# Performance work log

Hardware: AMD Instinct MI355X
Metric: run time of the kernel (lower is better)

The kernel has to match this reference:

```python
import jax, jax.numpy as jnp
import numpy as np

B, T, V, E, H, M, L = 64, 512, 32000, 256, 600, 600, 4


def _lstm_dir(x, Wih, Whh, b, reverse):
    # x: [T,B,Din]; PyTorch gate order i,f,g,o; b = b_ih + b_hh fused
    Hd = Whh.shape[1]
    Bn = x.shape[1]

    def step(carry, xt):
        h, c = carry
        g = xt @ Wih.T + h @ Whh.T + b
        i, f, gg, o = jnp.split(g, 4, axis=-1)
        c = jax.nn.sigmoid(f) * c + jax.nn.sigmoid(i) * jnp.tanh(gg)
        h = jax.nn.sigmoid(o) * jnp.tanh(c)
        return (h, c), h

    init = (jnp.zeros((Bn, Hd), x.dtype), jnp.zeros((Bn, Hd), x.dtype))
    _, hs = jax.lax.scan(step, init, x, reverse=reverse)
    return hs  # [T,B,H]


def _crf_log_likelihood(emissions, tags, transitions, start_trans, end_trans):
    # emissions [B,T,L], tags [B,T]; full-length mask
    emit_sc = jnp.take_along_axis(emissions, tags[..., None], axis=-1)[..., 0].sum(-1)
    trans_sc = transitions[tags[:, :-1], tags[:, 1:]].sum(-1)
    numerator = start_trans[tags[:, 0]] + emit_sc + trans_sc + end_trans[tags[:, -1]]

    alpha0 = start_trans[None, :] + emissions[:, 0]  # [B,L]

    def step(alpha, e_t):
        a = jax.nn.logsumexp(alpha[:, :, None] + transitions[None], axis=1) + e_t
        return a, None

    alpha, _ = jax.lax.scan(step, alpha0, jnp.swapaxes(emissions, 0, 1)[1:])
    denominator = jax.nn.logsumexp(alpha + end_trans[None, :], axis=1)
    return (numerator - denominator).sum()


def _viterbi(emissions, transitions, start_trans, end_trans):
    alpha0 = start_trans[None, :] + emissions[:, 0]

    def step(alpha, e_t):
        sc = alpha[:, :, None] + transitions[None]  # [B,L,L]
        bp = jnp.argmax(sc, axis=1)                 # [B,L]
        return jnp.max(sc, axis=1) + e_t, bp

    alpha, bps = jax.lax.scan(step, alpha0, jnp.swapaxes(emissions, 0, 1)[1:])
    last = jnp.argmax(alpha + end_trans[None, :], axis=1)  # [B]

    def back(tag, bp):
        prev = jnp.take_along_axis(bp, tag[:, None], axis=1)[:, 0]
        return prev, tag

    first, tags_rev = jax.lax.scan(back, last, bps, reverse=True)
    return jnp.concatenate([first[:, None], jnp.swapaxes(tags_rev, 0, 1)], axis=1)


def setup_inputs() -> dict:
    key = jax.random.key(0)
    ks = jax.random.split(key, 24)
    s = 0.05
    d = {}
    d['us'] = jax.random.randint(ks[0], (B, T), 0, V)
    d['ls'] = jax.random.randint(ks[1], (B, T), 0, L)
    d['embed'] = jax.random.normal(ks[2], (V, E), jnp.float32) * s
    # layer 0 (input E), layer 1 (input 2H); f=forward dir, b=backward dir
    d['Wih0f'] = jax.random.normal(ks[3], (4 * H, E), jnp.float32) * s
    d['Whh0f'] = jax.random.normal(ks[4], (4 * H, H), jnp.float32) * s
    d['b0f'] = jnp.zeros((4 * H,), jnp.float32)
    d['Wih0b'] = jax.random.normal(ks[5], (4 * H, E), jnp.float32) * s
    d['Whh0b'] = jax.random.normal(ks[6], (4 * H, H), jnp.float32) * s
    d['b0b'] = jnp.zeros((4 * H,), jnp.float32)
    d['Wih1f'] = jax.random.normal(ks[7], (4 * H, 2 * H), jnp.float32) * s
    d['Whh1f'] = jax.random.normal(ks[8], (4 * H, H), jnp.float32) * s
    d['b1f'] = jnp.zeros((4 * H,), jnp.float32)
    d['Wih1b'] = jax.random.normal(ks[9], (4 * H, 2 * H), jnp.float32) * s
    d['Whh1b'] = jax.random.normal(ks[10], (4 * H, H), jnp.float32) * s
    d['b1b'] = jnp.zeros((4 * H,), jnp.float32)
    d['W1'] = jax.random.normal(ks[11], (2 * H, M), jnp.float32) * s
    d['bm1'] = jnp.zeros((M,), jnp.float32)
    d['W2'] = jax.random.normal(ks[12], (M, L), jnp.float32) * s
    d['bm2'] = jnp.zeros((L,), jnp.float32)
    d['transitions'] = jax.random.normal(ks[13], (L, L), jnp.float32) * s
    d['start_trans'] = jax.random.normal(ks[14], (L,), jnp.float32) * s
    d['end_trans'] = jax.random.normal(ks[15], (L,), jnp.float32) * s
    return d


def reference(us, ls, embed, Wih0f, Whh0f, b0f, Wih0b, Whh0b, b0b,
              Wih1f, Whh1f, b1f, Wih1b, Whh1b, b1b,
              W1, bm1, W2, bm2, transitions, start_trans, end_trans):
    x = embed[us]                      # [B,T,E] embedding lookup (dropout p=0)
    x = jnp.swapaxes(x, 0, 1)          # [T,B,E]
    h0 = jnp.concatenate([
        _lstm_dir(x, Wih0f, Whh0f, b0f, False),
        _lstm_dir(x, Wih0b, Whh0b, b0b, True)], axis=-1)   # [T,B,2H]
    h1 = jnp.concatenate([
        _lstm_dir(h0, Wih1f, Whh1f, b1f, False),
        _lstm_dir(h0, Wih1b, Whh1b, b1b, True)], axis=-1)  # [T,B,2H]
    ys = (h1 @ W1 + bm1) @ W2 + bm2    # MLP with Identity activation -> [T,B,L]
    ys = jnp.swapaxes(ys, 0, 1)        # [B,T,L]
    ll = _crf_log_likelihood(ys, ls, transitions, start_trans, end_trans)
    loss = -ll / B
    tags = _viterbi(ys, transitions, start_trans, end_trans)
    return loss, tags
```

## Files before the change

### kernel.cpp

```cpp
#include <hip/hip_runtime.h>
#include <hip/hip_bf16.h>
#include <math.h>

#define T_ 512
#define B_ 64
#define E_ 256
#define H_ 600
#define G4 2400
#define MTOT 32768
#define NP 2432
#define KP1 1216
#define GSTR (38 * 19 * 512)
#define PARS (2 * 64 * 608)

typedef __attribute__((ext_vector_type(8))) short bf16x8;
typedef __attribute__((ext_vector_type(4))) float f32x4;

static __device__ __forceinline__ ushort f2bf(float x) {
    unsigned u = __builtin_bit_cast(unsigned, x);
    unsigned r = (u + 0x7FFFu + ((u >> 16) & 1u)) >> 16;
    return (ushort)r;
}
static __device__ __forceinline__ float bf2f(ushort h) {
    unsigned u = ((unsigned)h) << 16;
    return __builtin_bit_cast(float, u);
}

__global__ __launch_bounds__(256) void zero_kernel(float* __restrict__ p, int n) {
    int i = blockIdx.x * 256 + threadIdx.x;
    if (i < n) p[i] = 0.f;
}

__global__ __launch_bounds__(256) void xsplit(const int* __restrict__ us,
                                              const float* __restrict__ embed,
                                              ushort* __restrict__ xh) {
    int m = blockIdx.x;
    int t = m >> 6, b = m & 63;
    int tok = us[b * T_ + t];
    int k = threadIdx.x;
    float v = embed[(size_t)tok * E_ + k];
    xh[(size_t)m * E_ + k] = f2bf(v);
}

__global__ __launch_bounds__(256) void padzero(ushort* __restrict__ h) {
    int idx = blockIdx.x * 256 + threadIdx.x;
    int m = idx >> 4, c = 1200 + (idx & 15);
    h[(size_t)m * KP1 + c] = 0;
}

__global__ __launch_bounds__(512) void pack_wih(const float* __restrict__ Wf,
                                                const float* __restrict__ Wb, int K, int NKS,
                                                ushort* __restrict__ phF,
                                                ushort* __restrict__ phB) {
    int nb = blockIdx.x, ks = blockIdx.y, dz = blockIdx.z;
    const float* W = dz ? Wb : Wf;
    ushort* ph = dz ? phB : phF;
    int tid = threadIdx.x;
    int l = tid >> 3, e = tid & 7;
    int g = nb / 38, ub = nb % 38;
    int u = ub * 16 + (l & 15);
    int k = ks * 32 + (l >> 4) * 8 + e;
    float v = (u < 600 && k < K) ? W[(size_t)(g * 600 + u) * K + k] : 0.f;
    ph[((size_t)nb * NKS + ks) * 512 + tid] = f2bf(v);
}

__global__ __launch_bounds__(512) void pack_whh(
    const float* __restrict__ W0f, const float* __restrict__ W0b,
    const float* __restrict__ W1f, const float* __restrict__ W1b,
    ushort* __restrict__ pwh, ushort* __restrict__ pwl) {
    int ub = blockIdx.x, ks = blockIdx.y, ld = blockIdx.z;
    const float* W = (ld == 0) ? W0f : (ld == 1) ? W0b : (ld == 2) ? W1f : W1b;
    int tid = threadIdx.x;
    int l = tid >> 3, e = tid & 7;
    int u = ub * 16 + (l & 15);
    int k = ks * 32 + (l >> 4) * 8 + e;
#pragma unroll
    for (int g = 0; g < 4; ++g) {
        float v = (u < 600 && k < 600) ? W[(size_t)(g * 600 + u) * 600 + k] : 0.f;
        ushort hi = f2bf(v);
        size_t o = ((((size_t)ld * 4 + g) * 38 + ub) * 19 + ks) * 512 + tid;
        pwh[o] = hi;
        pwl[o] = f2bf(v - bf2f(hi));
    }
}

__global__ __launch_bounds__(64) void packbias(const float* __restrict__ b0f,
                                               const float* __restrict__ b0b,
                                               const float* __restrict__ b1f,
                                               const float* __restrict__ b1b,
                                               float* __restrict__ bfr) {
    int ub = blockIdx.x, g = blockIdx.y, ld = blockIdx.z;
    const float* b = (ld == 0) ? b0f : (ld == 1) ? b0b : (ld == 2) ? b1f : b1b;
    int lane = threadIdx.x;
    float4 v;
    float* vp = (float*)&v;
#pragma unroll
    for (int r = 0; r < 4; ++r) {
        int u = ub * 16 + (lane >> 4) * 4 + r;
        vp[r] = (u < 600) ? b[g * 600 + u] : 0.f;
    }
    *(float4*)&bfr[((((size_t)ld * 4 + g) * 38 + ub) * 64 + lane) * 4] = v;
}

__global__ void wc_kernel(const float* __restrict__ W1, const float* __restrict__ bm1,
                          const float* __restrict__ W2, const float* __restrict__ bm2,
                          float* __restrict__ Wc, float* __restrict__ bc) {
    int idx = blockIdx.x * 256 + threadIdx.x;
    if (idx < 4800) {
        int k = idx >> 2, l = idx & 3;
        float acc = 0.f;
        for (int j = 0; j < 600; ++j) acc += W1[(size_t)k * 600 + j] * W2[j * 4 + l];
        Wc[idx] = acc;
    }
    if (idx < 4) {
        float acc = bm2[idx];
        for (int j = 0; j < 600; ++j) acc += bm1[j] * W2[j * 4 + idx];
        bc[idx] = acc;
    }
}

#define LOADAG(Ah, KS)                                                           \
    _Pragma("unroll") for (int i = 0; i < 4; ++i) {                              \
        size_t o = ((size_t)(wn16 + i) * NKS + (KS)) * 512 + lane * 8;           \
        Ah[i] = *(const bf16x8*)(Aph + o);                                       \
    }
#define READB(BUF)                                                               \
    _Pragma("unroll") for (int j = 0; j < 4; ++j) {                              \
        bh[j] = *(const bf16x8*)&BsH[BUF][wm + j * 16 + fr][kb8];                \
    }
#define MFALL(Ah)                                                                \
    _Pragma("unroll") for (int i = 0; i < 4; ++i)                                \
        _Pragma("unroll") for (int j = 0; j < 4; ++j)                            \
            acc[i][j] = __builtin_amdgcn_mfma_f32_16x16x32_bf16(Ah[i], bh[j], acc[i][j], 0, 0, 0);

__global__ __launch_bounds__(256) void gemm_mfma(
    const ushort* __restrict__ AphF, const ushort* __restrict__ AphB,
    const ushort* __restrict__ actH,
    int Kp, int NKS, int m_offF, int m_offB,
    float* __restrict__ preF, float* __restrict__ preB) {
    __shared__ __align__(16) ushort BsH[2][128][40];
    const ushort* Aph = blockIdx.z ? AphB : AphF;
    float* preX = blockIdx.z ? preB : preF;
    int m_off = blockIdx.z ? m_offB : m_offF;
    int n0 = blockIdx.x * 128, m0 = blockIdx.y * 128;
    int tid = threadIdx.x, lane = tid & 63, w = tid >> 6;
    int wn16 = (n0 >> 4) + (w >> 1) * 4;
    int wm = (w & 1) * 64;
    int fr = lane & 15, kb8 = (lane >> 4) * 8;
    int srow = tid >> 1, skg = (tid & 1) * 16;
    const ushort* bHrow = actH + (size_t)(m_off + m0 + srow) * Kp + skg;

    uint4 rh0 = *(const uint4*)bHrow, rh1 = *(const uint4*)(bHrow + 8);

    bf16x8 a0h[4], a1h[4], bh[4];
    LOADAG(a0h, 0)

    f32x4 acc[4][4] = {};

    for (int ks = 0; ks < NKS; ks += 2) {
        *(uint4*)&BsH[0][srow][skg] = rh0;
        *(uint4*)&BsH[0][srow][skg + 8] = rh1;
        {
            const ushort* bh_ = bHrow + (ks + 1) * 32;
            rh0 = *(const uint4*)bh_; rh1 = *(const uint4*)(bh_ + 8);
        }
        LOADAG(a1h, ks + 1)
        __syncthreads();
        READB(0)
        MFALL(a0h)
        __syncthreads();
        *(uint4*)&BsH[1][srow][skg] = rh0;
        *(uint4*)&BsH[1][srow][skg + 8] = rh1;
        {
            int ksn = (ks + 2 < NKS) ? ks + 2 : 0;
            const ushort* bh_ = bHrow + ksn * 32;
            rh0 = *(const uint4*)bh_; rh1 = *(const uint4*)(bh_ + 8);
            LOADAG(a0h, ksn)
        }
        __syncthreads();
        READB(1)
        MFALL(a1h)
        __syncthreads();
    }

#pragma unroll
    for (int i = 0; i < 4; ++i) {
        int n16 = wn16 + i;
        int g = n16 / 38, ub = n16 - g * 38;
#pragma unroll
        for (int j = 0; j < 4; ++j) {
            int mloc = m0 + wm + j * 16;
            int tl = mloc >> 6, ntg = (mloc >> 4) & 3;
            float* dst = preX + (((((size_t)tl * 4 + g) * 38 + ub) * 4 + ntg) * 64 + lane) * 4;
            *(f32x4*)dst = acc[i][j];
        }
    }
}

#define LOADA(Ah, Al, KS)                                                        \
    _Pragma("unroll") for (int g = 0; g < 4; ++g) {                              \
        size_t o = (size_t)(dir * 4 + g) * GSTR + wub + (size_t)(KS)*512 + lane * 8; \
        Ah[g] = *(const bf16x8*)(pwh + o);                                       \
        Al[g] = *(const bf16x8*)(pwl + o);                                       \
    }
#define LOADB1(Bh, Bl, KS)                                                       \
    {                                                                            \
        size_t o = (size_t)(KS)*32 + fk8;                                        \
        Bh = *(const bf16x8*)(hHb + o);                                          \
        Bl = *(const bf16x8*)(hLb + o);                                          \
    }
#define MFT1(Aa, Bb)                                                             \
    _Pragma("unroll") for (int g = 0; g < 4; ++g)                                \
        acc[g] = __builtin_amdgcn_mfma_f32_16x16x32_bf16(Aa[g], Bb, acc[g], 0, 0, 0);
#define MF31(Ah, Al, Bh, Bl) MFT1(Ah, Bh) MFT1(Ah, Bl) MFT1(Al, Bh)

__global__ __launch_bounds__(256) void lstm_step_mfma(
    const ushort* __restrict__ pwh, const ushort* __restrict__ pwl,
    const ushort* __restrict__ hInH, const ushort* __restrict__ hInL,
    ushort* __restrict__ hOutH, ushort* __restrict__ hOutL,
    const float* __restrict__ preF2, const float* __restrict__ preB2,
    int tF, int tB,
    const float* __restrict__ biasFr, int layer,
    float* __restrict__ cQ,
    ushort* __restrict__ h0H, int mF, int mB,
    float* __restrict__ h1f, float* __restrict__ h1b, int oF, int oB, int chunkRows) {
    __shared__ float hsh[4][16][17];
    int tid = threadIdx.x;
    int lane = tid & 63, nt = tid >> 6;
    int blk = blockIdx.x;
    int dir = (blk >= 38) ? 1 : 0;
    int ub = blk - dir * 38;
    int u16 = ub * 16;
    int frow = lane & 15, rr = lane >> 4, fk8 = rr * 8;
    size_t wub = (size_t)ub * 9728;
    const ushort* hHb = hInH + ((size_t)dir * 64 + nt * 16 + frow) * 608;
    const ushort* hLb = hInL + ((size_t)dir * 64 + nt * 16 + frow) * 608;

    f32x4 acc[4] = {};
    bf16x8 A0h[4], A0l[4], A1h[4], A1l[4];
    bf16x8 B0h, B0l, B1h, B1l;

    LOADA(A0h, A0l, 0)
    LOADB1(B0h, B0l, 0)
    for (int ks = 0; ks < 18; ks += 2) {
        LOADA(A1h, A1l, ks + 1)
        LOADB1(B1h, B1l, ks + 1)
        MF31(A0h, A0l, B0h, B0l)
        LOADA(A0h, A0l, ks + 2)
        LOADB1(B0h, B0l, ks + 2)
        MF31(A1h, A1l, B1h, B1l)
    }
    MF31(A0h, A0l, B0h, B0l)

    const float* preX = dir ? preB2 : preF2;
    int t = dir ? tB : tF;
    float4 pg[4], bf4[4];
#pragma unroll
    for (int g = 0; g < 4; ++g) {
        pg[g] = *(const float4*)(preX + (((((size_t)t * 4 + g) * 38 + ub) * 4 + nt) * 64 + lane) * 4);
        bf4[g] = *(const float4*)(biasFr + ((((size_t)(layer * 2 + dir) * 4 + g) * 38 + ub) * 64 + lane) * 4);
    }
    int slot = (dir * 38 + ub) * 4 + nt;
    float* cslot = cQ + ((size_t)slot * 64 + lane) * 4;
    float4 cvec = *(float4*)cslot;
    float* cvp = (float*)&cvec;
#pragma unroll
    for (int r = 0; r < 4; ++r) {
        int u = u16 + rr * 4 + r;
        bool valid = (u < 600);
        float gi, gf, gg, go;
        if (valid) {
            gi = acc[0][r] + ((float*)&pg[0])[r] + ((float*)&bf4[0])[r];
            gf = acc[1][r] + ((float*)&pg[1])[r] + ((float*)&bf4[1])[r];
            gg = acc[2][r] + ((float*)&pg[2])[r] + ((float*)&bf4[2])[r];
            go = acc[3][r] + ((float*)&pg[3])[r] + ((float*)&bf4[3])[r];
        } else {
            gi = gf = gg = go = 0.f;
        }
        float cv = cvp[r];
        float si = 1.f / (1.f + expf(-gi));
        float sf = 1.f / (1.f + expf(-gf));
        float so = 1.f / (1.f + expf(-go));
        float cn = sf * cv + si * tanhf(gg);
        float hn = so * tanhf(cn);
        cvp[r] = cn;
        hsh[nt][frow][rr * 4 + r] = hn;
    }
    *(float4*)cslot = cvec;
    __syncthreads();

    {
        int bl = lane >> 2, q = lane & 3;
        int b = nt * 16 + bl;
        float v0 = hsh[nt][bl][q * 4 + 0], v1 = hsh[nt][bl][q * 4 + 1];
        float v2 = hsh[nt][bl][q * 4 + 2], v3 = hsh[nt][bl][q * 4 + 3];
        ushort h0_ = f2bf(v0), h1_ = f2bf(v1), h2_ = f2bf(v2), h3_ = f2bf(v3);
        ushort4 hv = {h0_, h1_, h2_, h3_};
        ushort4 lv = {f2bf(v0 - bf2f(h0_)), f2bf(v1 - bf2f(h1_)),
                      f2bf(v2 - bf2f(h2_)), f2bf(v3 - bf2f(h3_))};
        size_t ho = ((size_t)dir * 64 + b) * 608 + u16 + q * 4;
        *(ushort4*)&hOutH[ho] = hv;
        *(ushort4*)&hOutL[ho] = lv;
        if (layer == 0 && (u16 + q * 4 < 600)) {
            size_t so_ = (size_t)((dir ? mB : mF) + b) * KP1 + dir * 600 + u16 + q * 4;
            *(ushort4*)&h0H[so_] = hv;
        }
    }
    if (layer == 1) {
        int u_l = lane & 15, br = (lane >> 4) * 4;
        if (u16 + u_l < 600) {
            float4 hv;
            hv.x = hsh[nt][br + 0][u_l];
            hv.y = hsh[nt][br + 1][u_l];
            hv.z = hsh[nt][br + 2][u_l];
            hv.w = hsh[nt][br + 3][u_l];
            float* op = dir ? h1b : h1f;
            *(float4*)&op[(size_t)(u16 + u_l) * chunkRows + (dir ? oB : oF) + nt * 16 + br] = hv;
        }
    }
}

__global__ __launch_bounds__(256) void emis_add(const float* __restrict__ h1C, int cols,
                                                const float* __restrict__ Wc,
                                                const float* __restrict__ bc, int addBias,
                                                float* __restrict__ ys, int t0) {
    int lane = threadIdx.x & 63;
    int l = __builtin_amdgcn_readfirstlane(threadIdx.x >> 6);
    int tl = blockIdx.x;
    float acc = addBias ? bc[l] : 0.f;
    for (int k = 0; k < H_; ++k)
        acc = fmaf(h1C[(size_t)k * cols + tl * 64 + lane], Wc[k * 4 + l], acc);
    int t = t0 + tl, b = lane;
    ys[((size_t)b * T_ + t) * 4 + l] += acc;
}

__global__ void crf_fwd(const float* __restrict__ ys, const int* __restrict__ ls,
                        const float* __restrict__ trans, const float* __restrict__ startT,
                        const float* __restrict__ endT, float* __restrict__ llb) {
    int b = blockIdx.x;
    int lane = threadIdx.x;
    float acc = 0.f;
    for (int t = lane; t < T_; t += 64) {
        int tg = ls[b * T_ + t];
        acc += ys[((size_t)b * T_ + t) * 4 + tg];
        if (t > 0) acc += trans[ls[b * T_ + t - 1] * 4 + tg];
    }
    for (int off = 32; off; off >>= 1) acc += __shfl_down(acc, off);
    float num = 0.f;
    if (lane == 0) num = startT[ls[b * T_]] + acc + endT[ls[b * T_ + T_ - 1]];

    float a = -1e30f;
    if (lane < 4) a = startT[lane] + ys[((size_t)b * T_) * 4 + lane];
    for (int t = 1; t < T_; ++t) {
        float a0 = __shfl(a, 0), a1 = __shfl(a, 1), a2 = __shfl(a, 2), a3 = __shfl(a, 3);
        if (lane < 4) {
            float v0 = a0 + trans[0 * 4 + lane];
            float v1 = a1 + trans[1 * 4 + lane];
            float v2 = a2 + trans[2 * 4 + lane];
            float v3 = a3 + trans[3 * 4 + lane];
            float mx = fmaxf(fmaxf(v0, v1), fmaxf(v2, v3));
            float ssum = expf(v0 - mx) + expf(v1 - mx) + expf(v2 - mx) + expf(v3 - mx);
            a = mx + logf(ssum) + ys[((size_t)b * T_ + t) * 4 + lane];
        }
    }
    float a0 = __shfl(a, 0), a1 = __shfl(a, 1), a2 = __shfl(a, 2), a3 = __shfl(a, 3);
    if (lane == 0) {
        float v0 = a0 + endT[0], v1 = a1 + endT[1], v2 = a2 + endT[2], v3 = a3 + endT[3];
        float mx = fmaxf(fmaxf(v0, v1), fmaxf(v2, v3));
        float den = mx + logf(expf(v0 - mx) + expf(v1 - mx) + expf(v2 - mx) + expf(v3 - mx));
        llb[b] = num - den;
    }
}

__global__ void final_loss(const float* __restrict__ llb, float* __restrict__ out) {
    int lane = threadIdx.x;
    float v = llb[lane];
    for (int off = 32; off; off >>= 1) v += __shfl_down(v, off);
    if (lane == 0) out[0] = -v / 64.0f;
}

__global__ void viterbi(const float* __restrict__ ys, const float* __restrict__ trans,
                        const float* __restrict__ startT, const float* __restrict__ endT,
                        float* __restrict__ out) {
    __shared__ unsigned char bp[T_ * 4];
    int b = blockIdx.x;
    int lane = threadIdx.x;
    float a = -1e30f;
    if (lane < 4) a = startT[lane] + ys[((size_t)b * T_) * 4 + lane];
    for (int t = 1; t < T_; ++t) {
        float a0 = __shfl(a, 0), a1 = __shfl(a, 1), a2 = __shfl(a, 2), a3 = __shfl(a, 3);
        if (lane < 4) {
            float av[4] = {a0, a1, a2, a3};
            float best = av[0] + trans[lane];
            int bi = 0;
            for (int lp = 1; lp < 4; ++lp) {
                float v = av[lp] + trans[lp * 4 + lane];
                if (v > best) { best = v; bi = lp; }
            }
            bp[t * 4 + lane] = (unsigned char)bi;
            a = best + ys[((size_t)b * T_ + t) * 4 + lane];
        }
    }
    float a0 = __shfl(a, 0), a1 = __shfl(a, 1), a2 = __shfl(a, 2), a3 = __shfl(a, 3);
    if (lane == 0) {
        float v[4] = {a0 + endT[0], a1 + endT[1], a2 + endT[2], a3 + endT[3]};
        int tag = 0;
        float best = v[0];
        for (int l = 1; l < 4; ++l)
            if (v[l] > best) { best = v[l]; tag = l; }
        out[1 + b * T_ + (T_ - 1)] = (float)tag;
        for (int t = T_ - 1; t >= 1; --t) {
            tag = bp[t * 4 + tag];
            out[1 + b * T_ + t - 1] = (float)tag;
        }
    }
}

extern "C" void kernel_launch(void* const* d_in, const int* in_sizes, int n_in,
                              void* d_out, int out_size, void* d_ws, size_t ws_size,
                              hipStream_t stream) {
    const int* us = (const int*)d_in[0];
    const int* ls = (const int*)d_in[1];
    const float* embed = (const float*)d_in[2];
    const float* Wih0f = (const float*)d_in[3];
    const float* Whh0f = (const float*)d_in[4];
    const float* b0f   = (const float*)d_in[5];
    const float* Wih0b = (const float*)d_in[6];
    const float* Whh0b = (const float*)d_in[7];
    const float* b0b   = (const float*)d_in[8];
    const float* Wih1f = (const float*)d_in[9];
    const float* Whh1f = (const float*)d_in[10];
    const float* b1f   = (const float*)d_in[11];
    const float* Wih1b = (const float*)d_in[12];
    const float* Whh1b = (const float*)d_in[13];
    const float* b1b   = (const float*)d_in[14];
    const float* W1    = (const float*)d_in[15];
    const float* bm1   = (const float*)d_in[16];
    const float* W2    = (const float*)d_in[17];
    const float* bm2   = (const float*)d_in[18];
    const float* trans = (const float*)d_in[19];
    const float* startT= (const float*)d_in[20];
    const float* endT  = (const float*)d_in[21];
    float* out = (float*)d_out;

    char* p = (char*)d_ws;
    auto alloc = [&](size_t bytes) {
        char* r = p;
        p += (bytes + 255) & ~(size_t)255;
        return r;
    };
    ushort* xspH = (ushort*)alloc((size_t)MTOT * E_ * 2);
    ushort* h0spH = (ushort*)alloc((size_t)MTOT * KP1 * 2);
    ushort* pw0hf = (ushort*)alloc((size_t)152 * 8 * 512 * 2);
    ushort* pw0hb = (ushort*)alloc((size_t)152 * 8 * 512 * 2);
    ushort* pw1hf = (ushort*)alloc((size_t)152 * 38 * 512 * 2);
    ushort* pw1hb = (ushort*)alloc((size_t)152 * 38 * 512 * 2);
    ushort* pwh = (ushort*)alloc((size_t)16 * GSTR * 2);
    ushort* pwl = (ushort*)alloc((size_t)16 * GSTR * 2);
    ushort* hTh = (ushort*)alloc((size_t)2 * PARS * 2);
    ushort* hTl = (ushort*)alloc((size_t)2 * PARS * 2);
    float* cQ  = (float*)alloc((size_t)304 * 64 * 4 * 4);
    float* biasFr = (float*)alloc((size_t)4 * 4 * 38 * 64 * 4 * 4);
    float* Wc  = (float*)alloc(4800 * 4);
    float* bc  = (float*)alloc(4 * 4);
    float* ysb = (float*)alloc((size_t)B_ * T_ * 4 * 4);
    float* llb = (float*)alloc(64 * 4);

    size_t used = (size_t)(p - (char*)d_ws);
    size_t perTc = (size_t)2 * 2432 * 64 * 4 + (size_t)2 * H_ * 64 * 4;
    int Tc = 128;
    while (Tc > 8 && used + (size_t)Tc * perTc + 4096 > ws_size) Tc >>= 1;
    float* preF = (float*)alloc((size_t)Tc * 2432 * 64 * 4);
    float* preB = (float*)alloc((size_t)Tc * 2432 * 64 * 4);
    float* h1fC = (float*)alloc((size_t)H_ * Tc * 64 * 4);
    float* h1bC = (float*)alloc((size_t)H_ * Tc * 64 * 4);
    int nc = T_ / Tc;
    int chunkRows = Tc * 64;

    xsplit<<<MTOT, 256, 0, stream>>>(us, embed, xspH);
    pack_wih<<<dim3(152, 8, 2), 512, 0, stream>>>(Wih0f, Wih0b, E_, 8, pw0hf, pw0hb);
    pack_wih<<<dim3(152, 38, 2), 512, 0, stream>>>(Wih1f, Wih1b, 1200, 38, pw1hf, pw1hb);
    pack_whh<<<dim3(38, 19, 4), 512, 0, stream>>>(Whh0f, Whh0b, Whh1f, Whh1b, pwh, pwl);
    packbias<<<dim3(38, 4, 4), 64, 0, stream>>>(b0f, b0b, b1f, b1b, biasFr);
    padzero<<<(MTOT * 16) / 256, 256, 0, stream>>>(h0spH);
    wc_kernel<<<19, 256, 0, stream>>>(W1, bm1, W2, bm2, Wc, bc);
    zero_kernel<<<(B_ * T_ * 4 + 255) / 256, 256, 0, stream>>>(ysb, B_ * T_ * 4);

    for (int layer = 0; layer < 2; ++layer) {
        int Kp = layer ? KP1 : E_;
        int NKS = Kp / 32;
        const ushort* aH = layer ? h0spH : xspH;
        const ushort* AphF = layer ? pw1hf : pw0hf;
        const ushort* AphB = layer ? pw1hb : pw0hb;
        const ushort* pwhL = pwh + (size_t)layer * 8 * GSTR;
        const ushort* pwlL = pwl + (size_t)layer * 8 * GSTR;

        zero_kernel<<<(PARS + 255) / 256, 256, 0, stream>>>((float*)hTh, PARS);
        zero_kernel<<<(PARS + 255) / 256, 256, 0, stream>>>((float*)hTl, PARS);
        zero_kernel<<<(304 * 64 * 4 + 255) / 256, 256, 0, stream>>>(cQ, 304 * 64 * 4);

        for (int c = 0; c < nc; ++c) {
            int moffF = c * Tc * 64;
            int moffB = (T_ - (c + 1) * Tc) * 64;
            dim3 gg(NP / 128, chunkRows / 128, 2);
            gemm_mfma<<<gg, 256, 0, stream>>>(AphF, AphB, aH, Kp, NKS, moffF, moffB,
                                              preF, preB);
            for (int s = 0; s < Tc; ++s) {
                int step = c * Tc + s;
                int par = step & 1;
                lstm_step_mfma<<<76, 256, 0, stream>>>(
                    pwhL, pwlL,
                    hTh + (size_t)par * PARS, hTl + (size_t)par * PARS,
                    hTh + (size_t)(par ^ 1) * PARS, hTl + (size_t)(par ^ 1) * PARS,
                    preF, preB, s, Tc - 1 - s,
                    biasFr, layer, cQ,
                    h0spH, step * 64, (T_ - 1 - step) * 64,
                    h1fC, h1bC, s * 64, (Tc - 1 - s) * 64, chunkRows);
            }
            if (layer == 1) {
                emis_add<<<Tc, 256, 0, stream>>>(h1fC, chunkRows, Wc, bc, 1, ysb, c * Tc);
                emis_add<<<Tc, 256, 0, stream>>>(h1bC, chunkRows, Wc + 600 * 4, bc, 0, ysb,
                                                 T_ - (c + 1) * Tc);
            }
        }
    }

    crf_fwd<<<B_, 64, 0, stream>>>(ysb, ls, trans, startT, endT, llb);
    final_loss<<<1, 64, 0, stream>>>(llb, out);
    viterbi<<<B_, 64, 0, stream>>>(ysb, trans, startT, endT, out);
}
```

Measured before the change: 15.02 ms.

## Fuse per-step LSTM launches into a persistent cooperative kernel with LDS-resident weights

Replaces the one-launch-per-timestep LSTM recurrence with a single cooperative kernel per chunk. It loops over timesteps and separates them with grid.sync, and it loads each block's recurrent weight slice into shared memory once instead of re-reading it from global memory every step. The cell state stays in registers across the chunk, and the MFMA loop gets a deeper software-pipelined prefetch. The aim is to remove kernel launch overhead and repeated weight traffic. The cost is heavy LDS use (about 150KB per block) and grid-wide barrier latency, which requires all 76 blocks to be co-resident.

```diff
diff --git a/kernel.cpp b/kernel.cpp
--- a/kernel.cpp
+++ b/kernel.cpp
@@ -1,6 +1,9 @@
 #include <hip/hip_runtime.h>
 #include <hip/hip_bf16.h>
+#include <hip/hip_cooperative_groups.h>
 #include <math.h>
+
+namespace cg = cooperative_groups;
 
 #define T_ 512
 #define B_ 64
@@ -197,34 +200,37 @@
     }
 }
 
-#define LOADA(Ah, Al, KS)                                                        \
+#define CC_LOADA(SL, KS)                                                         \
     _Pragma("unroll") for (int g = 0; g < 4; ++g) {                              \
-        size_t o = (size_t)(dir * 4 + g) * GSTR + wub + (size_t)(KS)*512 + lane * 8; \
-        Ah[g] = *(const bf16x8*)(pwh + o);                                       \
-        Al[g] = *(const bf16x8*)(pwl + o);                                       \
-    }
-#define LOADB1(Bh, Bl, KS)                                                       \
+        Ah[SL][g] = *(const bf16x8*)&wlds[0][g][(size_t)(KS)*512 + lane * 8];    \
+        Al[SL][g] = *(const bf16x8*)&wlds[1][g][(size_t)(KS)*512 + lane * 8];    \
+    }
+#define CC_LOADB(SL, KS)                                                         \
     {                                                                            \
-        size_t o = (size_t)(KS)*32 + fk8;                                        \
-        Bh = *(const bf16x8*)(hHb + o);                                          \
-        Bl = *(const bf16x8*)(hLb + o);                                          \
-    }
-#define MFT1(Aa, Bb)                                                             \
+        Bh[SL] = *(const bf16x8*)(hHb + (size_t)(KS)*32 + fk8);                  \
+        Bl[SL] = *(const bf16x8*)(hLb + (size_t)(KS)*32 + fk8);                  \
+    }
+#define CC_MF3(SA, SB)                                                           \
     _Pragma("unroll") for (int g = 0; g < 4; ++g)                                \
-        acc[g] = __builtin_amdgcn_mfma_f32_16x16x32_bf16(Aa[g], Bb, acc[g], 0, 0, 0);
-#define MF31(Ah, Al, Bh, Bl) MFT1(Ah, Bh) MFT1(Ah, Bl) MFT1(Al, Bh)
-
-__global__ __launch_bounds__(256) void lstm_step_mfma(
+        acc[g] = __builtin_amdgcn_mfma_f32_16x16x32_bf16(Ah[SA][g], Bh[SB], acc[g], 0, 0, 0); \
+    _Pragma("unroll") for (int g = 0; g < 4; ++g)                                \
+        acc[g] = __builtin_amdgcn_mfma_f32_16x16x32_bf16(Ah[SA][g], Bl[SB], acc[g], 0, 0, 0); \
+    _Pragma("unroll") for (int g = 0; g < 4; ++g)                                \
+        acc[g] = __builtin_amdgcn_mfma_f32_16x16x32_bf16(Al[SA][g], Bh[SB], acc[g], 0, 0, 0);
+
+__global__ __launch_bounds__(256, 1) void lstm_chunk_coop(
     const ushort* __restrict__ pwh, const ushort* __restrict__ pwl,
-    const ushort* __restrict__ hInH, const ushort* __restrict__ hInL,
-    ushort* __restrict__ hOutH, ushort* __restrict__ hOutL,
+    ushort* __restrict__ hTh, ushort* __restrict__ hTl,
     const float* __restrict__ preF2, const float* __restrict__ preB2,
-    int tF, int tB,
+    int Tc, int step0,
     const float* __restrict__ biasFr, int layer,
     float* __restrict__ cQ,
-    ushort* __restrict__ h0H, int mF, int mB,
-    float* __restrict__ h1f, float* __restrict__ h1b, int oF, int oB, int chunkRows) {
+    ushort* __restrict__ h0H,
+    float* __restrict__ h1f, float* __restrict__ h1b, int chunkRows) {
+    __shared__ ushort wlds[2][4][19 * 512];
     __shared__ float hsh[4][16][17];
+    cg::grid_group grid = cg::this_grid();
+
     int tid = threadIdx.x;
     int lane = tid & 63, nt = tid >> 6;
     int blk = blockIdx.x;
@@ -232,92 +238,120 @@
     int ub = blk - dir * 38;
     int u16 = ub * 16;
     int frow = lane & 15, rr = lane >> 4, fk8 = rr * 8;
-    size_t wub = (size_t)ub * 9728;
-    const ushort* hHb = hInH + ((size_t)dir * 64 + nt * 16 + frow) * 608;
-    const ushort* hLb = hInL + ((size_t)dir * 64 + nt * 16 + frow) * 608;
-
-    f32x4 acc[4] = {};
-    bf16x8 A0h[4], A0l[4], A1h[4], A1l[4];
-    bf16x8 B0h, B0l, B1h, B1l;
-
-    LOADA(A0h, A0l, 0)
-    LOADB1(B0h, B0l, 0)
-    for (int ks = 0; ks < 18; ks += 2) {
-        LOADA(A1h, A1l, ks + 1)
-        LOADB1(B1h, B1l, ks + 1)
-        MF31(A0h, A0l, B0h, B0l)
-        LOADA(A0h, A0l, ks + 2)
-        LOADB1(B0h, B0l, ks + 2)
-        MF31(A1h, A1l, B1h, B1l)
-    }
-    MF31(A0h, A0l, B0h, B0l)
+
+#pragma unroll
+    for (int g = 0; g < 4; ++g) {
+        const uint4* sH = (const uint4*)(pwh + (size_t)(dir * 4 + g) * GSTR + (size_t)ub * 9728);
+        const uint4* sL = (const uint4*)(pwl + (size_t)(dir * 4 + g) * GSTR + (size_t)ub * 9728);
+        uint4* dH = (uint4*)&wlds[0][g][0];
+        uint4* dL = (uint4*)&wlds[1][g][0];
+        for (int i = tid; i < 1216; i += 256) {
+            dH[i] = sH[i];
+            dL[i] = sL[i];
+        }
+    }
 
     const float* preX = dir ? preB2 : preF2;
-    int t = dir ? tB : tF;
-    float4 pg[4], bf4[4];
-#pragma unroll
-    for (int g = 0; g < 4; ++g) {
-        pg[g] = *(const float4*)(preX + (((((size_t)t * 4 + g) * 38 + ub) * 4 + nt) * 64 + lane) * 4);
+    float4 bf4[4];
+#pragma unroll
+    for (int g = 0; g < 4; ++g)
         bf4[g] = *(const float4*)(biasFr + ((((size_t)(layer * 2 + dir) * 4 + g) * 38 + ub) * 64 + lane) * 4);
-    }
+
     int slot = (dir * 38 + ub) * 4 + nt;
     float* cslot = cQ + ((size_t)slot * 64 + lane) * 4;
     float4 cvec = *(float4*)cslot;
     float* cvp = (float*)&cvec;
-#pragma unroll
-    for (int r = 0; r < 4; ++r) {
-        int u = u16 + rr * 4 + r;
-        bool valid = (u < 600);
-        float gi, gf, gg, go;
-        if (valid) {
-            gi = acc[0][r] + ((float*)&pg[0])[r] + ((float*)&bf4[0])[r];
-            gf = acc[1][r] + ((float*)&pg[1])[r] + ((float*)&bf4[1])[r];
-            gg = acc[2][r] + ((float*)&pg[2])[r] + ((float*)&bf4[2])[r];
-            go = acc[3][r] + ((float*)&pg[3])[r] + ((float*)&bf4[3])[r];
-        } else {
-            gi = gf = gg = go = 0.f;
-        }
-        float cv = cvp[r];
-        float si = 1.f / (1.f + expf(-gi));
-        float sf = 1.f / (1.f + expf(-gf));
-        float so = 1.f / (1.f + expf(-go));
-        float cn = sf * cv + si * tanhf(gg);
-        float hn = so * tanhf(cn);
-        cvp[r] = cn;
-        hsh[nt][frow][rr * 4 + r] = hn;
+    __syncthreads();
+
+    for (int s = 0; s < Tc; ++s) {
+        int par = (step0 + s) & 1;
+        const ushort* hHb = hTh + (size_t)par * PARS + ((size_t)dir * 64 + nt * 16 + frow) * 608;
+        const ushort* hLb = hTl + (size_t)par * PARS + ((size_t)dir * 64 + nt * 16 + frow) * 608;
+        int t = dir ? (Tc - 1 - s) : s;
+
+        float4 pg[4];
+#pragma unroll
+        for (int g = 0; g < 4; ++g)
+            pg[g] = *(const float4*)(preX + (((((size_t)t * 4 + g) * 38 + ub) * 4 + nt) * 64 + lane) * 4);
+
+        f32x4 acc[4] = {};
+        bf16x8 Ah[3][4], Al[3][4], Bh[6], Bl[6];
+        CC_LOADB(0, 0) CC_LOADB(1, 1) CC_LOADB(2, 2)
+        CC_LOADB(3, 3) CC_LOADB(4, 4) CC_LOADB(5, 5)
+        CC_LOADA(0, 0) CC_LOADA(1, 1)
+#pragma unroll
+        for (int ks = 0; ks < 19; ++ks) {
+            const int ca = ks % 3, cb = ks % 6;
+            if (ks + 2 < 19) {
+                const int pa = (ks + 2) % 3;
+                CC_LOADA(pa, ks + 2)
+            }
+            if (ks + 6 < 19) {
+                const int pb = (ks + 6) % 6;
+                CC_LOADB(pb, ks + 6)
+            }
+            CC_MF3(ca, cb)
+        }
+
+#pragma unroll
+        for (int r = 0; r < 4; ++r) {
+            int u = u16 + rr * 4 + r;
+            bool valid = (u < 600);
+            float gi, gf, gg, go;
+            if (valid) {
+                gi = acc[0][r] + ((float*)&pg[0])[r] + ((float*)&bf4[0])[r];
+                gf = acc[1][r] + ((float*)&pg[1])[r] + ((float*)&bf4[1])[r];
+                gg = acc[2][r] + ((float*)&pg[2])[r] + ((float*)&bf4[2])[r];
+                go = acc[3][r] + ((float*)&pg[3])[r] + ((float*)&bf4[3])[r];
+            } else {
+                gi = gf = gg = go = 0.f;
+            }
+            float cv = cvp[r];
+            float si = 1.f / (1.f + expf(-gi));
+            float sf = 1.f / (1.f + expf(-gf));
+            float so = 1.f / (1.f + expf(-go));
+            float cn = sf * cv + si * tanhf(gg);
+            float hn = so * tanhf(cn);
+            cvp[r] = cn;
+            hsh[nt][frow][rr * 4 + r] = hn;
+        }
+        __syncthreads();
+        {
+            int step = step0 + s;
+            int mF = step * 64, mB = (T_ - 1 - step) * 64;
+            int bl = lane >> 2, q = lane & 3;
+            int b = nt * 16 + bl;
+            float v0 = hsh[nt][bl][q * 4 + 0], v1 = hsh[nt][bl][q * 4 + 1];
+            float v2 = hsh[nt][bl][q * 4 + 2], v3 = hsh[nt][bl][q * 4 + 3];
+            ushort h0_ = f2bf(v0), h1_ = f2bf(v1), h2_ = f2bf(v2), h3_ = f2bf(v3);
+            ushort4 hv = {h0_, h1_, h2_, h3_};
+            ushort4 lv = {f2bf(v0 - bf2f(h0_)), f2bf(v1 - bf2f(h1_)),
+                          f2bf(v2 - bf2f(h2_)), f2bf(v3 - bf2f(h3_))};
+            size_t ho = (size_t)(par ^ 1) * PARS + ((size_t)dir * 64 + b) * 608 + u16 + q * 4;
+            *(ushort4*)&hTh[ho] = hv;
+            *(ushort4*)&hTl[ho] = lv;
+            if (layer == 0 && (u16 + q * 4 < 600)) {
+                size_t so_ = (size_t)((dir ? mB : mF) + b) * KP1 + dir * 600 + u16 + q * 4;
+                *(ushort4*)&h0H[so_] = hv;
+            }
+        }
+        if (layer == 1) {
+            int oF = s * 64, oB = (Tc - 1 - s) * 64;
+            int u_l = lane & 15, br = (lane >> 4) * 4;
+            if (u16 + u_l < 600) {
+                float4 hv;
+                hv.x = hsh[nt][br + 0][u_l];
+                hv.y = hsh[nt][br + 1][u_l];
+                hv.z = hsh[nt][br + 2][u_l];
+                hv.w = hsh[nt][br + 3][u_l];
+                float* op = dir ? h1b : h1f;
+                *(float4*)&op[(size_t)(u16 + u_l) * chunkRows + (dir ? oB : oF) + nt * 16 + br] = hv;
+            }
+        }
+        __syncthreads();
+        if (s != Tc - 1) grid.sync();
     }
     *(float4*)cslot = cvec;
-    __syncthreads();
-
-    {
-        int bl = lane >> 2, q = lane & 3;
-        int b = nt * 16 + bl;
-        float v0 = hsh[nt][bl][q * 4 + 0], v1 = hsh[nt][bl][q * 4 + 1];
-        float v2 = hsh[nt][bl][q * 4 + 2], v3 = hsh[nt][bl][q * 4 + 3];
-        ushort h0_ = f2bf(v0), h1_ = f2bf(v1), h2_ = f2bf(v2), h3_ = f2bf(v3);
-        ushort4 hv = {h0_, h1_, h2_, h3_};
-        ushort4 lv = {f2bf(v0 - bf2f(h0_)), f2bf(v1 - bf2f(h1_)),
-                      f2bf(v2 - bf2f(h2_)), f2bf(v3 - bf2f(h3_))};
-        size_t ho = ((size_t)dir * 64 + b) * 608 + u16 + q * 4;
-        *(ushort4*)&hOutH[ho] = hv;
-        *(ushort4*)&hOutL[ho] = lv;
-        if (layer == 0 && (u16 + q * 4 < 600)) {
-            size_t so_ = (size_t)((dir ? mB : mF) + b) * KP1 + dir * 600 + u16 + q * 4;
-            *(ushort4*)&h0H[so_] = hv;
-        }
-    }
-    if (layer == 1) {
-        int u_l = lane & 15, br = (lane >> 4) * 4;
-        if (u16 + u_l < 600) {
-            float4 hv;
-            hv.x = hsh[nt][br + 0][u_l];
-            hv.y = hsh[nt][br + 1][u_l];
-            hv.z = hsh[nt][br + 2][u_l];
-            hv.w = hsh[nt][br + 3][u_l];
-            float* op = dir ? h1b : h1f;
-            *(float4*)&op[(size_t)(u16 + u_l) * chunkRows + (dir ? oB : oF) + nt * 16 + br] = hv;
-        }
-    }
 }
 
 __global__ __launch_bounds__(256) void emis_add(const float* __restrict__ h1C, int cols,
@@ -505,17 +539,21 @@
             dim3 gg(NP / 128, chunkRows / 128, 2);
             gemm_mfma<<<gg, 256, 0, stream>>>(AphF, AphB, aH, Kp, NKS, moffF, moffB,
                                               preF, preB);
-            for (int s = 0; s < Tc; ++s) {
-                int step = c * Tc + s;
-                int par = step & 1;
-                lstm_step_mfma<<<76, 256, 0, stream>>>(
-                    pwhL, pwlL,
-                    hTh + (size_t)par * PARS, hTl + (size_t)par * PARS,
-                    hTh + (size_t)(par ^ 1) * PARS, hTl + (size_t)(par ^ 1) * PARS,
-                    preF, preB, s, Tc - 1 - s,
-                    biasFr, layer, cQ,
-                    h0spH, step * 64, (T_ - 1 - step) * 64,
-                    h1fC, h1bC, s * 64, (Tc - 1 - s) * 64, chunkRows);
+            {
+                int step0 = c * Tc;
+                const ushort* a0 = pwhL; const ushort* a1 = pwlL;
+                ushort* a2 = hTh; ushort* a3 = hTl;
+                const float* a4 = preF; const float* a5 = preB;
+                int a6 = Tc; int a7 = step0;
+                const float* a8 = biasFr; int a9 = layer;
+                float* a10 = cQ;
+                ushort* a11 = h0spH;
+                float* a12 = h1fC; float* a13 = h1bC;
+                int a14 = chunkRows;
+                void* args[15] = {&a0, &a1, &a2, &a3, &a4, &a5, &a6, &a7,
+                                  &a8, &a9, &a10, &a11, &a12, &a13, &a14};
+                hipLaunchCooperativeKernel((void*)lstm_chunk_coop, dim3(76), dim3(256),
+                                           args, 0, stream);
             }
             if (layer == 1) {
                 emis_add<<<Tc, 256, 0, stream>>>(h1fC, chunkRows, Wc, bc, 1, ysb, c * Tc);
```

New measurement: 19.40 ms. 1.29x slower.

## Store LSTM input-projection and layer-1 outputs in bf16, enlarge chunk size

Applied to the files above, without the earlier changes.

The input-projection GEMM now writes its pre-activations as bf16 instead of fp32, and the LSTM step reads them back as bf16. Layer-1 hidden outputs are also stored as bf16 for the emission kernel. Halving these buffers lets the time chunk grow up to 512, which cuts the number of GEMM launches. The pre-activation and c-state loads are hoisted ahead of the recurrent MFMA loop, and three zeroing launches are merged into one. The cost is reduced precision in the gate pre-activations and emissions, which could shift Viterbi tags.

```diff
diff --git a/kernel.cpp b/kernel.cpp
--- a/kernel.cpp
+++ b/kernel.cpp
@@ -29,6 +29,14 @@
 __global__ __launch_bounds__(256) void zero_kernel(float* __restrict__ p, int n) {
     int i = blockIdx.x * 256 + threadIdx.x;
     if (i < n) p[i] = 0.f;
+}
+
+__global__ __launch_bounds__(256) void zero3(float* __restrict__ a, float* __restrict__ b,
+                                             float* __restrict__ c) {
+    int i = blockIdx.x * 256 + threadIdx.x;
+    a[i] = 0.f;
+    b[i] = 0.f;
+    c[i] = 0.f;
 }
 
 __global__ __launch_bounds__(256) void xsplit(const int* __restrict__ us,
@@ -137,10 +145,10 @@
     const ushort* __restrict__ AphF, const ushort* __restrict__ AphB,
     const ushort* __restrict__ actH,
     int Kp, int NKS, int m_offF, int m_offB,
-    float* __restrict__ preF, float* __restrict__ preB) {
+    ushort* __restrict__ preF, ushort* __restrict__ preB) {
     __shared__ __align__(16) ushort BsH[2][128][40];
     const ushort* Aph = blockIdx.z ? AphB : AphF;
-    float* preX = blockIdx.z ? preB : preF;
+    ushort* preX = blockIdx.z ? preB : preF;
     int m_off = blockIdx.z ? m_offB : m_offF;
     int n0 = blockIdx.x * 128, m0 = blockIdx.y * 128;
     int tid = threadIdx.x, lane = tid & 63, w = tid >> 6;
@@ -191,8 +199,13 @@
         for (int j = 0; j < 4; ++j) {
             int mloc = m0 + wm + j * 16;
             int tl = mloc >> 6, ntg = (mloc >> 4) & 3;
-            float* dst = preX + (((((size_t)tl * 4 + g) * 38 + ub) * 4 + ntg) * 64 + lane) * 4;
-            *(f32x4*)dst = acc[i][j];
+            ushort* dst = preX + (((((size_t)tl * 4 + g) * 38 + ub) * 4 + ntg) * 64 + lane) * 4;
+            ushort4 o;
+            o.x = f2bf(acc[i][j][0]);
+            o.y = f2bf(acc[i][j][1]);
+            o.z = f2bf(acc[i][j][2]);
+            o.w = f2bf(acc[i][j][3]);
+            *(ushort4*)dst = o;
         }
     }
 }
@@ -218,12 +231,12 @@
     const ushort* __restrict__ pwh, const ushort* __restrict__ pwl,
     const ushort* __restrict__ hInH, const ushort* __restrict__ hInL,
     ushort* __restrict__ hOutH, ushort* __restrict__ hOutL,
-    const float* __restrict__ preF2, const float* __restrict__ preB2,
+    const ushort* __restrict__ preF2, const ushort* __restrict__ preB2,
     int tF, int tB,
     const float* __restrict__ biasFr, int layer,
     float* __restrict__ cQ,
     ushort* __restrict__ h0H, int mF, int mB,
-    float* __restrict__ h1f, float* __restrict__ h1b, int oF, int oB, int chunkRows) {
+    ushort* __restrict__ h1f, ushort* __restrict__ h1b, int oF, int oB, int chunkRows) {
     __shared__ float hsh[4][16][17];
     int tid = threadIdx.x;
     int lane = tid & 63, nt = tid >> 6;
@@ -236,6 +249,22 @@
     const ushort* hHb = hInH + ((size_t)dir * 64 + nt * 16 + frow) * 608;
     const ushort* hLb = hInL + ((size_t)dir * 64 + nt * 16 + frow) * 608;
 
+    const ushort* preX = dir ? preB2 : preF2;
+    int t = dir ? tB : tF;
+    ushort4 pgu[4];
+    float4 bf4[4];
+#pragma unroll
+    for (int g = 0; g < 4; ++g) {
+        pgu[g] = *(const ushort4*)(preX +
+            (((((size_t)t * 4 + g) * 38 + ub) * 4 + nt) * 64 + lane) * 4);
+        bf4[g] = *(const float4*)(biasFr +
+            ((((size_t)(layer * 2 + dir) * 4 + g) * 38 + ub) * 64 + lane) * 4);
+    }
+    int slot = (dir * 38 + ub) * 4 + nt;
+    float* cslot = cQ + ((size_t)slot * 64 + lane) * 4;
+    float4 cvec = *(float4*)cslot;
+    float* cvp = (float*)&cvec;
+
     f32x4 acc[4] = {};
     bf16x8 A0h[4], A0l[4], A1h[4], A1l[4];
     bf16x8 B0h, B0l, B1h, B1l;
@@ -252,28 +281,18 @@
     }
     MF31(A0h, A0l, B0h, B0l)
 
-    const float* preX = dir ? preB2 : preF2;
-    int t = dir ? tB : tF;
-    float4 pg[4], bf4[4];
-#pragma unroll
-    for (int g = 0; g < 4; ++g) {
-        pg[g] = *(const float4*)(preX + (((((size_t)t * 4 + g) * 38 + ub) * 4 + nt) * 64 + lane) * 4);
-        bf4[g] = *(const float4*)(biasFr + ((((size_t)(layer * 2 + dir) * 4 + g) * 38 + ub) * 64 + lane) * 4);
-    }
-    int slot = (dir * 38 + ub) * 4 + nt;
-    float* cslot = cQ + ((size_t)slot * 64 + lane) * 4;
-    float4 cvec = *(float4*)cslot;
-    float* cvp = (float*)&cvec;
 #pragma unroll
     for (int r = 0; r < 4; ++r) {
         int u = u16 + rr * 4 + r;
         bool valid = (u < 600);
         float gi, gf, gg, go;
         if (valid) {
-            gi = acc[0][r] + ((float*)&pg[0])[r] + ((float*)&bf4[0])[r];
-            gf = acc[1][r] + ((float*)&pg[1])[r] + ((float*)&bf4[1])[r];
-            gg = acc[2][r] + ((float*)&pg[2])[r] + ((float*)&bf4[2])[r];
-            go = acc[3][r] + ((float*)&pg[3])[r] + ((float*)&bf4[3])[r];
+            const ushort* pp = (const ushort*)&pgu[0];
+            gi = acc[0][r] + bf2f(((const ushort*)&pgu[0])[r]) + ((float*)&bf4[0])[r];
+            gf = acc[1][r] + bf2f(((const ushort*)&pgu[1])[r]) + ((float*)&bf4[1])[r];
+            gg = acc[2][r] + bf2f(((const ushort*)&pgu[2])[r]) + ((float*)&bf4[2])[r];
+            go = acc[3][r] + bf2f(((const ushort*)&pgu[3])[r]) + ((float*)&bf4[3])[r];
+            (void)pp;
         } else {
             gi = gf = gg = go = 0.f;
         }
@@ -309,18 +328,18 @@
     if (layer == 1) {
         int u_l = lane & 15, br = (lane >> 4) * 4;
         if (u16 + u_l < 600) {
-            float4 hv;
-            hv.x = hsh[nt][br + 0][u_l];
-            hv.y = hsh[nt][br + 1][u_l];
-            hv.z = hsh[nt][br + 2][u_l];
-            hv.w = hsh[nt][br + 3][u_l];
-            float* op = dir ? h1b : h1f;
-            *(float4*)&op[(size_t)(u16 + u_l) * chunkRows + (dir ? oB : oF) + nt * 16 + br] = hv;
-        }
-    }
-}
-
-__global__ __launch_bounds__(256) void emis_add(const float* __restrict__ h1C, int cols,
+            ushort4 hv4;
+            hv4.x = f2bf(hsh[nt][br + 0][u_l]);
+            hv4.y = f2bf(hsh[nt][br + 1][u_l]);
+            hv4.z = f2bf(hsh[nt][br + 2][u_l]);
+            hv4.w = f2bf(hsh[nt][br + 3][u_l]);
+            ushort* op = dir ? h1b : h1f;
+            *(ushort4*)&op[(size_t)(u16 + u_l) * chunkRows + (dir ? oB : oF) + nt * 16 + br] = hv4;
+        }
+    }
+}
+
+__global__ __launch_bounds__(256) void emis_add(const ushort* __restrict__ h1C, int cols,
                                                 const float* __restrict__ Wc,
                                                 const float* __restrict__ bc, int addBias,
                                                 float* __restrict__ ys, int t0) {
@@ -329,7 +348,7 @@
     int tl = blockIdx.x;
     float acc = addBias ? bc[l] : 0.f;
     for (int k = 0; k < H_; ++k)
-        acc = fmaf(h1C[(size_t)k * cols + tl * 64 + lane], Wc[k * 4 + l], acc);
+        acc = fmaf(bf2f(h1C[(size_t)k * cols + tl * 64 + lane]), Wc[k * 4 + l], acc);
     int t = t0 + tl, b = lane;
     ys[((size_t)b * T_ + t) * 4 + l] += acc;
 }
@@ -467,13 +486,13 @@
     float* llb = (float*)alloc(64 * 4);
 
     size_t used = (size_t)(p - (char*)d_ws);
-    size_t perTc = (size_t)2 * 2432 * 64 * 4 + (size_t)2 * H_ * 64 * 4;
-    int Tc = 128;
+    size_t perTc = (size_t)2 * 2432 * 64 * 2 + (size_t)2 * H_ * 64 * 2;
+    int Tc = 512;
     while (Tc > 8 && used + (size_t)Tc * perTc + 4096 > ws_size) Tc >>= 1;
-    float* preF = (float*)alloc((size_t)Tc * 2432 * 64 * 4);
-    float* preB = (float*)alloc((size_t)Tc * 2432 * 64 * 4);
-    float* h1fC = (float*)alloc((size_t)H_ * Tc * 64 * 4);
-    float* h1bC = (float*)alloc((size_t)H_ * Tc * 64 * 4);
+    ushort* preF = (ushort*)alloc((size_t)Tc * 2432 * 64 * 2);
+    ushort* preB = (ushort*)alloc((size_t)Tc * 2432 * 64 * 2);
+    ushort* h1fC = (ushort*)alloc((size_t)H_ * Tc * 64 * 2);
+    ushort* h1bC = (ushort*)alloc((size_t)H_ * Tc * 64 * 2);
     int nc = T_ / Tc;
     int chunkRows = Tc * 64;
 
@@ -495,9 +514,7 @@
         const ushort* pwhL = pwh + (size_t)layer * 8 * GSTR;
         const ushort* pwlL = pwl + (size_t)layer * 8 * GSTR;
 
-        zero_kernel<<<(PARS + 255) / 256, 256, 0, stream>>>((float*)hTh, PARS);
-        zero_kernel<<<(PARS + 255) / 256, 256, 0, stream>>>((float*)hTl, PARS);
-        zero_kernel<<<(304 * 64 * 4 + 255) / 256, 256, 0, stream>>>(cQ, 304 * 64 * 4);
+        zero3<<<PARS / 256, 256, 0, stream>>>((float*)hTh, (float*)hTl, cQ);
 
         for (int c = 0; c < nc; ++c) {
             int moffF = c * Tc * 64;
```

New measurement: 14.03 ms. -6.6%, faster.
